# Performance work log

Hardware: AMD Instinct MI355X
Metric: run time of the kernel (lower is better)

Reference implementation:

```python
import jax, jax.numpy as jnp
import numpy as np
from jax import lax


def _rnn_scan(x, Wih, Whh, bih, bhh):
    """Elman RNN: h_t = tanh(x_t @ Wih^T + bih + h_{t-1} @ Whh^T + bhh).
    x: (B, T, I). Returns (last_hidden (B,H), all_hidden (B,T,H))."""
    B = x.shape[0]
    H = Whh.shape[0]
    xs = jnp.swapaxes(x, 0, 1)  # (T, B, I)
    h0 = jnp.zeros((B, H), dtype=x.dtype)

    def step(h, xt):
        h_new = jnp.tanh(xt @ Wih.T + bih + h @ Whh.T + bhh)
        return h_new, h_new

    last, hs = lax.scan(step, h0, xs)
    return last, jnp.swapaxes(hs, 0, 1)  # (B,H), (B,T,H)


def setup_inputs() -> dict:
    key = jax.random.key(0)
    ks = jax.random.split(key, 12)
    B, T = 4096, 256
    I1, H1, H2 = 1, 5, 100
    s1 = 1.0 / np.sqrt(H1)
    s2 = 1.0 / np.sqrt(H2)
    inp = {
        "x": jax.random.normal(ks[0], (B, T, I1), dtype=jnp.float32),
        "Wih1": jax.random.uniform(ks[1], (H1, I1), jnp.float32, -s1, s1),
        "Whh1": jax.random.uniform(ks[2], (H1, H1), jnp.float32, -s1, s1),
        "bih1": jax.random.uniform(ks[3], (H1,), jnp.float32, -s1, s1),
        "bhh1": jax.random.uniform(ks[4], (H1,), jnp.float32, -s1, s1),
        "Wih2": jax.random.uniform(ks[5], (H2, H1), jnp.float32, -s2, s2),
        "Whh2": jax.random.uniform(ks[6], (H2, H2), jnp.float32, -s2, s2),
        "bih2": jax.random.uniform(ks[7], (H2,), jnp.float32, -s2, s2),
        "bhh2": jax.random.uniform(ks[8], (H2,), jnp.float32, -s2, s2),
        "W3": jax.random.uniform(ks[9], (1, H2), jnp.float32, -s2, s2),
        "b3": jax.random.uniform(ks[10], (1,), jnp.float32, -s2, s2),
    }
    return inp


def reference(x, Wih1, Whh1, bih1, bhh1, Wih2, Whh2, bih2, bhh2, W3, b3):
    # layer_1: out = last hidden (B,5), hidden = full sequence (B,T,5)
    _, h1_seq = _rnn_scan(x, Wih1, Whh1, bih1, bhh1)
    # layer_2 consumes the hidden sequence of layer_1
    out2, _ = _rnn_scan(h1_seq, Wih2, Whh2, bih2, bhh2)  # (B,100)
    # final linear + relu
    return jax.nn.relu(out2 @ W3.T + b3)  # (B,1)
```

## Files before the change

### kernel.cpp

```cpp
#include <hip/hip_runtime.h>
#include <stdint.h>

#define T_STEPS 256
#define H1 5
#define H2 100
#define NSTR 16
#define MT 7
#define KT 4
#define ME 112
#define KE 128
#define XPAD 260
#define NW 7
#define NTHR (NW * 64)

typedef _Float16 f16;
typedef _Float16 half8 __attribute__((ext_vector_type(8)));
typedef _Float16 f16x2 __attribute__((ext_vector_type(2)));
typedef float    floatx4 __attribute__((ext_vector_type(4)));

__device__ __forceinline__ int sidx(int k, int n) {
    return ((k >> 5) << 9) + (((k >> 3) & 3) << 7) + (n << 3) + (k & 7);
}

__device__ __forceinline__ float fast_tanh(float v) {
    float e = __expf(2.0f * v);
    return 1.0f - 2.0f * __builtin_amdgcn_rcpf(e + 1.0f);
}

__device__ __forceinline__ uint32_t pkf16(float a, float b) {
    f16x2 v; v.x = (f16)a; v.y = (f16)b;
    return __builtin_bit_cast(uint32_t, v);
}

__global__ __launch_bounds__(NTHR, 1) void rnn_mfma7p(
    const float* __restrict__ x,
    const float* __restrict__ Wih1, const float* __restrict__ Whh1,
    const float* __restrict__ bih1, const float* __restrict__ bhh1,
    const float* __restrict__ Wih2, const float* __restrict__ Whh2,
    const float* __restrict__ bih2, const float* __restrict__ bhh2,
    const float* __restrict__ W3,   const float* __restrict__ b3,
    float* __restrict__ out)
{
    const int tid  = threadIdx.x;
    const int lane = tid & 63;
    const int wid  = tid >> 6;
    const int n    = lane & 15;
    const int g    = lane >> 4;
    const int bbase = blockIdx.x * NSTR;

    __shared__ __align__(16) f16   Wlds[ME][KE];
    __shared__ __align__(16) float xs[NSTR][XPAD];
    __shared__ __align__(16) f16   st[2][2048];
    __shared__ float pp[NW][NSTR];

    {
        uint32_t* w32 = (uint32_t*)&Wlds[0][0];
        #pragma unroll
        for (int i = 0; i < 16; ++i) w32[tid + NTHR * i] = 0u;
        const float4* xg = (const float4*)(x + (size_t)bbase * T_STEPS);
        for (int gi = tid; gi < 1024; gi += NTHR)
            *(float4*)&xs[gi >> 6][4 * (gi & 63)] = xg[gi];
    }
    __syncthreads();
    for (int i = tid; i < H2 * H2; i += NTHR) Wlds[i / H2][i % H2] = (f16)Whh2[i];
    for (int i = tid; i < H2 * H1; i += NTHR) Wlds[i / H1][H2 + i % H1] = (f16)Wih2[i];
    for (int i = tid; i < H2; i += NTHR)      Wlds[i][105] = (f16)(bih2[i] + bhh2[i]);
    if (tid < H1 * H1) Wlds[H2 + tid / H1][H2 + tid % H1] = (f16)Whh1[tid];
    if (tid < H1) {
        Wlds[H2 + tid][105] = (f16)(bih1[tid] + bhh1[tid]);
        Wlds[H2 + tid][106] = (f16)Wih1[tid];
    }
    {
        uint32_t* s32 = (uint32_t*)&st[0][0];
        for (int i = tid; i < 2 * 2048 / 2; i += NTHR) s32[i] = 0u;
    }
    __syncthreads();
    if (tid < NSTR) {
        const float x0 = xs[tid][0];
        #pragma unroll
        for (int c = 0; c < H1; ++c)
            st[0][sidx(H2 + c, tid)] = (f16)fast_tanh(Wih1[c] * x0 + bih1[c] + bhh1[c]);
        st[0][sidx(105, tid)] = (f16)1.0f;
        st[0][sidx(106, tid)] = (f16)xs[tid][1];
    }
    half8 Af[KT];
    #pragma unroll
    for (int kt = 0; kt < KT; ++kt)
        Af[kt] = *(const half8*)&Wlds[16 * wid + n][32 * kt + 8 * g];
    __syncthreads();

    const int roff = 16 * lane;
    const int woff = ((wid >> 1) << 10) + (((2 * wid + (g >> 1)) & 3) << 8)
                   + (n << 4) + ((g & 1) << 3);
    const char* const sp0 = (const char*)&st[0][0];
    char*       const sp1 = (char*)&st[1][0];

    auto fullstep = [&](const char* rp, char* wp, int t) {
        float xv = 0.0f;
        if (wid == 6) {
            const int xi = (t + 2 < T_STEPS) ? (t + 2) : (T_STEPS - 1);
            xv = xs[n][xi];
        }
        half8 Bf[KT];
        #pragma unroll
        for (int kt = 0; kt < KT; ++kt)
            Bf[kt] = *(const half8*)(rp + roff + 1024 * kt);

        __builtin_amdgcn_s_setprio(1);
        floatx4 Da = {0.f, 0.f, 0.f, 0.f}, Db = {0.f, 0.f, 0.f, 0.f};
        Da = __builtin_amdgcn_mfma_f32_16x16x32_f16(Af[0], Bf[0], Da, 0, 0, 0);
        Db = __builtin_amdgcn_mfma_f32_16x16x32_f16(Af[2], Bf[2], Db, 0, 0, 0);
        Da = __builtin_amdgcn_mfma_f32_16x16x32_f16(Af[1], Bf[1], Da, 0, 0, 0);
        Db = __builtin_amdgcn_mfma_f32_16x16x32_f16(Af[3], Bf[3], Db, 0, 0, 0);
        const floatx4 D = Da + Db;

        uint32_t q0 = pkf16(fast_tanh(D[0]), fast_tanh(D[1]));
        uint32_t q1 = pkf16(fast_tanh(D[2]), fast_tanh(D[3]));
        if (wid == 6) {
            if (g == 2) {
                q0 = pkf16(fast_tanh(D[0]), 1.0f);
                q1 = pkf16(xv, 0.0f);
            } else if (g == 3) { q0 = 0u; q1 = 0u; }
        }
        __builtin_amdgcn_s_setprio(0);

        uint2 w; w.x = q0; w.y = q1;
        *(uint2*)(wp + woff) = w;
        __syncthreads();
    };

    #pragma unroll 1
    for (int t2 = 0; t2 < T_STEPS - 2; t2 += 2) {
        fullstep(sp0, sp1, t2);
        fullstep(sp1, (char*)sp0, t2 + 1);
    }
    fullstep(sp0, sp1, T_STEPS - 2);

    uint32_t P0, P1;
    {
        half8 Bf[KT];
        #pragma unroll
        for (int kt = 0; kt < KT; ++kt)
            Bf[kt] = *(const half8*)(sp1 + roff + 1024 * kt);
        floatx4 Da = {0.f, 0.f, 0.f, 0.f}, Db = {0.f, 0.f, 0.f, 0.f};
        Da = __builtin_amdgcn_mfma_f32_16x16x32_f16(Af[0], Bf[0], Da, 0, 0, 0);
        Db = __builtin_amdgcn_mfma_f32_16x16x32_f16(Af[2], Bf[2], Db, 0, 0, 0);
        Da = __builtin_amdgcn_mfma_f32_16x16x32_f16(Af[1], Bf[1], Da, 0, 0, 0);
        Db = __builtin_amdgcn_mfma_f32_16x16x32_f16(Af[3], Bf[3], Db, 0, 0, 0);
        const floatx4 D = Da + Db;
        P0 = pkf16(fast_tanh(D[0]), fast_tanh(D[1]));
        P1 = pkf16(fast_tanh(D[2]), fast_tanh(D[3]));
    }

    float p = 0.0f;
    {
        const int mbase = 16 * wid + 4 * g;
        if (mbase < H2) {
            const float4 w3v = *(const float4*)(W3 + mbase);
            const f16x2 lo = __builtin_bit_cast(f16x2, P0);
            const f16x2 hi = __builtin_bit_cast(f16x2, P1);
            p += w3v.x * (float)lo.x + w3v.y * (float)lo.y
               + w3v.z * (float)hi.x + w3v.w * (float)hi.y;
        }
    }
    p += __shfl_xor(p, 16);
    p += __shfl_xor(p, 32);
    if (lane < NSTR) pp[wid][n] = p;
    __syncthreads();
    if (tid < NSTR) {
        float s = b3[0];
        #pragma unroll
        for (int w = 0; w < NW; ++w) s += pp[w][tid];
        out[bbase + tid] = fmaxf(s, 0.0f);
    }
}

extern "C" void kernel_launch(void* const* d_in, const int* in_sizes, int n_in,
                              void* d_out, int out_size, void* d_ws, size_t ws_size,
                              hipStream_t stream) {
    const float* x    = (const float*)d_in[0];
    const float* Wih1 = (const float*)d_in[1];
    const float* Whh1 = (const float*)d_in[2];
    const float* bih1 = (const float*)d_in[3];
    const float* bhh1 = (const float*)d_in[4];
    const float* Wih2 = (const float*)d_in[5];
    const float* Whh2 = (const float*)d_in[6];
    const float* bih2 = (const float*)d_in[7];
    const float* bhh2 = (const float*)d_in[8];
    const float* W3   = (const float*)d_in[9];
    const float* b3   = (const float*)d_in[10];
    float* out = (float*)d_out;

    const int B = in_sizes[0] / T_STEPS;
    rnn_mfma7p<<<B / NSTR, NTHR, 0, stream>>>(x, Wih1, Whh1, bih1, bhh1,
                                              Wih2, Whh2, bih2, bhh2, W3, b3, out);
}
```

Before: 96.81 us.

## Add dedicated eighth wave to stream x inputs into recurrent state buffer

Adds an eighth wavefront whose only job is to write the next x_t value into the shared-memory state buffer each step, taking part in the same barriers as the compute waves. The MFMA waves no longer load x or do per-wave special-case packing. Wave 6 now writes only the layer-1 h value for row 104. The bias-ones column is preset once in both buffers. The aim is to shorten the per-step critical path, at the cost of barriers that span more waves and an extra writer to the state buffer.

Result: faster. 83.90 us, median of 2 (-13.3%).

```diff
diff --git a/kernel.cpp b/kernel.cpp
--- a/kernel.cpp
+++ b/kernel.cpp
@@ -10,7 +10,7 @@
 #define ME 112
 #define KE 128
 #define XPAD 260
-#define NW 7
+#define NW 8
 #define NTHR (NW * 64)
 
 typedef _Float16 f16;
@@ -32,7 +32,7 @@
     return __builtin_bit_cast(uint32_t, v);
 }
 
-__global__ __launch_bounds__(NTHR, 1) void rnn_mfma7p(
+__global__ __launch_bounds__(NTHR, 1) void rnn_mfma8(
     const float* __restrict__ x,
     const float* __restrict__ Wih1, const float* __restrict__ Whh1,
     const float* __restrict__ bih1, const float* __restrict__ bhh1,
@@ -56,10 +56,13 @@
     {
         uint32_t* w32 = (uint32_t*)&Wlds[0][0];
         #pragma unroll
-        for (int i = 0; i < 16; ++i) w32[tid + NTHR * i] = 0u;
+        for (int i = 0; i < 14; ++i) w32[tid + NTHR * i] = 0u;
         const float4* xg = (const float4*)(x + (size_t)bbase * T_STEPS);
-        for (int gi = tid; gi < 1024; gi += NTHR)
+        #pragma unroll
+        for (int i = 0; i < 2; ++i) {
+            const int gi = tid + NTHR * i;
             *(float4*)&xs[gi >> 6][4 * (gi & 63)] = xg[gi];
+        }
     }
     __syncthreads();
     for (int i = tid; i < H2 * H2; i += NTHR) Wlds[i / H2][i % H2] = (f16)Whh2[i];
@@ -72,7 +75,8 @@
     }
     {
         uint32_t* s32 = (uint32_t*)&st[0][0];
-        for (int i = tid; i < 2 * 2048 / 2; i += NTHR) s32[i] = 0u;
+        #pragma unroll
+        for (int i = 0; i < 4; ++i) s32[tid + NTHR * i] = 0u;
     }
     __syncthreads();
     if (tid < NSTR) {
@@ -81,63 +85,75 @@
         for (int c = 0; c < H1; ++c)
             st[0][sidx(H2 + c, tid)] = (f16)fast_tanh(Wih1[c] * x0 + bih1[c] + bhh1[c]);
         st[0][sidx(105, tid)] = (f16)1.0f;
+        st[1][sidx(105, tid)] = (f16)1.0f;
         st[0][sidx(106, tid)] = (f16)xs[tid][1];
     }
     half8 Af[KT];
-    #pragma unroll
-    for (int kt = 0; kt < KT; ++kt)
-        Af[kt] = *(const half8*)&Wlds[16 * wid + n][32 * kt + 8 * g];
+    if (wid < MT) {
+        #pragma unroll
+        for (int kt = 0; kt < KT; ++kt)
+            Af[kt] = *(const half8*)&Wlds[16 * wid + n][32 * kt + 8 * g];
+    }
     __syncthreads();
 
     const int roff = 16 * lane;
     const int woff = ((wid >> 1) << 10) + (((2 * wid + (g >> 1)) & 3) << 8)
                    + (n << 4) + ((g & 1) << 3);
-    const char* const sp0 = (const char*)&st[0][0];
-    char*       const sp1 = (char*)&st[1][0];
-
-    auto fullstep = [&](const char* rp, char* wp, int t) {
-        float xv = 0.0f;
-        if (wid == 6) {
-            const int xi = (t + 2 < T_STEPS) ? (t + 2) : (T_STEPS - 1);
-            xv = xs[n][xi];
-        }
-        half8 Bf[KT];
-        #pragma unroll
-        for (int kt = 0; kt < KT; ++kt)
-            Bf[kt] = *(const half8*)(rp + roff + 1024 * kt);
-
-        __builtin_amdgcn_s_setprio(1);
-        floatx4 Da = {0.f, 0.f, 0.f, 0.f}, Db = {0.f, 0.f, 0.f, 0.f};
-        Da = __builtin_amdgcn_mfma_f32_16x16x32_f16(Af[0], Bf[0], Da, 0, 0, 0);
-        Db = __builtin_amdgcn_mfma_f32_16x16x32_f16(Af[2], Bf[2], Db, 0, 0, 0);
-        Da = __builtin_amdgcn_mfma_f32_16x16x32_f16(Af[1], Bf[1], Da, 0, 0, 0);
-        Db = __builtin_amdgcn_mfma_f32_16x16x32_f16(Af[3], Bf[3], Db, 0, 0, 0);
-        const floatx4 D = Da + Db;
-
-        uint32_t q0 = pkf16(fast_tanh(D[0]), fast_tanh(D[1]));
-        uint32_t q1 = pkf16(fast_tanh(D[2]), fast_tanh(D[3]));
-        if (wid == 6) {
-            if (g == 2) {
-                q0 = pkf16(fast_tanh(D[0]), 1.0f);
-                q1 = pkf16(xv, 0.0f);
-            } else if (g == 3) { q0 = 0u; q1 = 0u; }
-        }
-        __builtin_amdgcn_s_setprio(0);
-
-        uint2 w; w.x = q0; w.y = q1;
-        *(uint2*)(wp + woff) = w;
+    char* const sp0 = (char*)&st[0][0];
+    char* const sp1 = (char*)&st[1][0];
+    uint32_t P0 = 0u, P1 = 0u;
+
+    if (wid == 7) {
+        f16* const w0 = &st[0][0];
+        f16* const w1 = &st[1][0];
+        const int si = sidx(106, n);
+        #pragma unroll 1
+        for (int t2 = 0; t2 < T_STEPS - 2; t2 += 2) {
+            if (lane < NSTR) w1[si] = (f16)xs[n][t2 + 2];
+            __syncthreads();
+            if (lane < NSTR) w0[si] = (f16)xs[n][t2 + 3 < T_STEPS ? t2 + 3 : T_STEPS - 1];
+            __syncthreads();
+        }
+        if (lane < NSTR) w1[si] = (f16)xs[n][T_STEPS - 1];
         __syncthreads();
-    };
-
-    #pragma unroll 1
-    for (int t2 = 0; t2 < T_STEPS - 2; t2 += 2) {
-        fullstep(sp0, sp1, t2);
-        fullstep(sp1, (char*)sp0, t2 + 1);
-    }
-    fullstep(sp0, sp1, T_STEPS - 2);
-
-    uint32_t P0, P1;
-    {
+    } else {
+        auto fullstep = [&](const char* rp, char* wp) {
+            half8 Bf[KT];
+            #pragma unroll
+            for (int kt = 0; kt < KT; ++kt)
+                Bf[kt] = *(const half8*)(rp + roff + 1024 * kt);
+
+            __builtin_amdgcn_s_setprio(1);
+            floatx4 Da = {0.f, 0.f, 0.f, 0.f}, Db = {0.f, 0.f, 0.f, 0.f};
+            Da = __builtin_amdgcn_mfma_f32_16x16x32_f16(Af[0], Bf[0], Da, 0, 0, 0);
+            Db = __builtin_amdgcn_mfma_f32_16x16x32_f16(Af[2], Bf[2], Db, 0, 0, 0);
+            Da = __builtin_amdgcn_mfma_f32_16x16x32_f16(Af[1], Bf[1], Da, 0, 0, 0);
+            Db = __builtin_amdgcn_mfma_f32_16x16x32_f16(Af[3], Bf[3], Db, 0, 0, 0);
+            const floatx4 D = Da + Db;
+
+            if (wid < 6 || g < 2) {
+                const uint32_t q0 = pkf16(fast_tanh(D[0]), fast_tanh(D[1]));
+                const uint32_t q1 = pkf16(fast_tanh(D[2]), fast_tanh(D[3]));
+                __builtin_amdgcn_s_setprio(0);
+                uint2 w; w.x = q0; w.y = q1;
+                *(uint2*)(wp + woff) = w;
+            } else if (g == 2) {
+                const f16 h4 = (f16)fast_tanh(D[0]);
+                __builtin_amdgcn_s_setprio(0);
+                *(f16*)(wp + 2 * (1664 + 8 * n)) = h4;
+            } else {
+                __builtin_amdgcn_s_setprio(0);
+            }
+            __syncthreads();
+        };
+
+        #pragma unroll 1
+        for (int t2 = 0; t2 < T_STEPS - 2; t2 += 2) {
+            fullstep(sp0, sp1);
+            fullstep(sp1, sp0);
+        }
+        fullstep(sp0, sp1);
+
         half8 Bf[KT];
         #pragma unroll
         for (int kt = 0; kt < KT; ++kt)
@@ -153,7 +169,7 @@
     }
 
     float p = 0.0f;
-    {
+    if (wid < MT) {
         const int mbase = 16 * wid + 4 * g;
         if (mbase < H2) {
             const float4 w3v = *(const float4*)(W3 + mbase);
@@ -170,7 +186,7 @@
     if (tid < NSTR) {
         float s = b3[0];
         #pragma unroll
-        for (int w = 0; w < NW; ++w) s += pp[w][tid];
+        for (int w = 0; w < MT; ++w) s += pp[w][tid];
         out[bbase + tid] = fmaxf(s, 0.0f);
     }
 }
@@ -192,6 +208,6 @@
     float* out = (float*)d_out;
 
     const int B = in_sizes[0] / T_STEPS;
-    rnn_mfma7p<<<B / NSTR, NTHR, 0, stream>>>(x, Wih1, Whh1, bih1, bhh1,
-                                              Wih2, Whh2, bih2, bhh2, W3, b3, out);
-}
+    rnn_mfma8<<<B / NSTR, NTHR, 0, stream>>>(x, Wih1, Whh1, bih1, bhh1,
+                                             Wih2, Whh2, bih2, bhh2, W3, b3, out);
+}
```
